# Kernel optimization log

Hardware: AMD Instinct MI355X
Metric: run time of the kernel (lower is better)

## Reference

```python
import jax, jax.numpy as jnp
import numpy as np

# Module constants from init_kwargs
A, T, HID, H, EGO = 50, 50, 128, 32, 0
C = 4 * HID // H   # per-head out channels = 16
B = 32
NEG_SLOPE = 0.2    # PyG GATConv default negative_slope


def setup_inputs() -> dict:
    key = jax.random.key(0)
    k1, k2, k3, k4 = jax.random.split(key, 4)
    h = jax.random.normal(k1, (B, A, T, HID), dtype=jnp.float32)
    # GATConv params: lin.weight (H*C, HID), att_src/att_dst (H, C), bias (H*C,)
    W = jax.random.normal(k2, (H * C, HID), dtype=jnp.float32) * (1.0 / np.sqrt(HID))
    att_src = jax.random.normal(k3, (H, C), dtype=jnp.float32) * 0.1
    att_dst = jax.random.normal(k4, (H, C), dtype=jnp.float32) * 0.1
    bias = jnp.zeros((H * C,), dtype=jnp.float32)
    return {"h": h, "W": W, "att_src": att_src, "att_dst": att_dst, "bias": bias}


def reference(h, W, att_src, att_dst, bias):
    # h: (B, A, T, HID). Node id = t*A + a after permute, matching build_ego_star_edges.
    b = h.shape[0]
    x = jnp.transpose(h, (0, 2, 1, 3))                       # (B, T, A, HID)
    # Linear projection into heads: (B, T, A, H, C)
    xw = jnp.einsum('btad,hcd->btahc', x, W.reshape(H, C, HID))
    a_src = jnp.einsum('btahc,hc->btah', xw, att_src)        # per-node src logit
    a_dst = jnp.einsum('btahc,hc->btah', xw, att_dst)        # per-node dst logit

    # Star topology: every (t_src, a != EGO) node -> every (t_dst, EGO) node.
    ne = jnp.array([a for a in range(A) if a != EGO])        # (A-1,) non-ego agents
    S = T * (A - 1)                                          # neighbors per ego dst
    x_ne = xw[:, :, ne].reshape(b, S, H, C)                  # (B, S, H, C)
    a_src_ne = a_src[:, :, ne].reshape(b, S, H)              # (B, S, H)
    a_dst_ego = a_dst[:, :, EGO]                             # (B, T, H)

    # Per-edge attention logits, segment-softmax over the S neighbors of each dst.
    logits = jax.nn.leaky_relu(a_src_ne[:, None, :, :] + a_dst_ego[:, :, None, :],
                               negative_slope=NEG_SLOPE)     # (B, T, S, H)
    att = jax.nn.softmax(logits, axis=2)

    # Weighted aggregation: (B, T, H, C) -> flatten heads (concat=True)
    out_ego = jnp.einsum('btsh,bshc->bthc', att, x_ne).reshape(b, T, H * C)

    # Nodes with no incoming edges get zero aggregation; bias added to all.
    out = jnp.zeros((b, T, A, H * C), dtype=h.dtype).at[:, :, EGO].set(out_ego)
    out = out + bias
    return jnp.transpose(out, (0, 2, 1, 3))                  # (B, A, T, H*C)
```

## Files before the change

kernel.cpp:

```cpp
#include <hip/hip_runtime.h>
#include <math.h>

#define NA    50
#define NT    50
#define HIDK  128
#define NH    32
#define NC    16
#define NB    32
#define SAT   2500
#define NS    2450
#define NOUT  512

__global__ __launch_bounds__(256) void k0_pq(const float* __restrict__ W,
                                             const float* __restrict__ att_src,
                                             const float* __restrict__ att_dst,
                                             float* __restrict__ PQ) {
  int g = blockIdx.x * 256 + threadIdx.x;
  int j = g >> 7, k = g & 127;
  int hh = j & 31;
  const float* att = (j < 32) ? att_src : att_dst;
  float acc = 0.f;
  #pragma unroll
  for (int c = 0; c < 16; ++c)
    acc = fmaf(att[hh * 16 + c], W[(size_t)(hh * 16 + c) * 128 + k], acc);
  PQ[g] = acc;
}

__global__ __launch_bounds__(256) void k1_ud(
    const float* __restrict__ X,
    const float* __restrict__ PQ,
    float* __restrict__ u,
    float* __restrict__ dv)
{
  __shared__ float Ast[32][68];
  __shared__ float Bst[32][68];
  const int tid = threadIdx.x;
  const int m0 = blockIdx.x * 64;
  const int ty = tid >> 4, tx = tid & 15;
  float acc[4][4] = {};
  const int sr = tid >> 3, sc = tid & 7;

  for (int kc = 0; kc < 128; kc += 32) {
    #pragma unroll
    for (int L = 0; L < 2; ++L) {
      int row = sr + L * 32;
      float4 v = *(const float4*)&X[(size_t)(m0 + row) * 128 + kc + sc * 4];
      Ast[sc*4+0][row] = v.x; Ast[sc*4+1][row] = v.y;
      Ast[sc*4+2][row] = v.z; Ast[sc*4+3][row] = v.w;
      float4 w = *(const float4*)&PQ[(size_t)row * 128 + kc + sc * 4];
      Bst[sc*4+0][row] = w.x; Bst[sc*4+1][row] = w.y;
      Bst[sc*4+2][row] = w.z; Bst[sc*4+3][row] = w.w;
    }
    __syncthreads();
    #pragma unroll
    for (int k = 0; k < 32; ++k) {
      float4 a4 = *(const float4*)&Ast[k][ty * 4];
      float4 b4 = *(const float4*)&Bst[k][tx * 4];
      float a[4] = {a4.x, a4.y, a4.z, a4.w};
      float bb[4] = {b4.x, b4.y, b4.z, b4.w};
      #pragma unroll
      for (int i = 0; i < 4; ++i)
        #pragma unroll
        for (int j = 0; j < 4; ++j)
          acc[i][j] = fmaf(a[i], bb[j], acc[i][j]);
    }
    __syncthreads();
  }

  #pragma unroll
  for (int i = 0; i < 4; ++i) {
    int m = m0 + ty * 4 + i;
    int b = m / SAT, s = m - b * SAT;
    #pragma unroll
    for (int jj = 0; jj < 4; ++jj) {
      int col = tx * 4 + jj;
      if (col < 32)
        u[(size_t)(b * 32 + col) * SAT + s] = acc[i][jj];
      else if (s < NT)
        dv[(size_t)(b * 32 + col - 32) * NT + s] = acc[i][jj];
    }
  }
}

#define LOADG(B_, g_) do {                                                  \
    _Pragma("unroll")                                                       \
    for (int j = 0; j < 4; ++j) {                                           \
      int idx_ = base + 2 * ((g_) * 4 + j);                                 \
      e##B_[j] = sE[idx_]; s##B_[j] = sIdx[idx_];                           \
    }                                                                       \
    _Pragma("unroll")                                                       \
    for (int j = 0; j < 4; ++j)                                             \
      x##B_[j] = *(const float4*)(xb + (size_t)s##B_[j] * HIDK);            \
  } while (0)

#define COMPG(B_) do {                                                      \
    _Pragma("unroll")                                                       \
    for (int j = 0; j < 4; ++j) {                                           \
      float2 ee = e##B_[j]; float4 xx = x##B_[j];                           \
      a1[0]=fmaf(ee.x,xx.x,a1[0]); a1[1]=fmaf(ee.x,xx.y,a1[1]);             \
      a1[2]=fmaf(ee.x,xx.z,a1[2]); a1[3]=fmaf(ee.x,xx.w,a1[3]);             \
      a2[0]=fmaf(ee.y,xx.x,a2[0]); a2[1]=fmaf(ee.y,xx.y,a2[1]);             \
      a2[2]=fmaf(ee.y,xx.z,a2[2]); a2[3]=fmaf(ee.y,xx.w,a2[3]);             \
      z1 += ee.x; z2 += ee.y;                                               \
    }                                                                       \
  } while (0)

__global__ __launch_bounds__(512, 4) void k2_attn(
    const float* __restrict__ X,
    const float* __restrict__ u,
    const float* __restrict__ dv,
    const float* __restrict__ W,
    const float* __restrict__ bias,
    float* __restrict__ out)
{
  const int id = blockIdx.x;
  const int b  = (id & 7) + 8 * (id >> 8);
  const int h  = (id >> 3) & 31;
  const int tid = threadIdx.x;

  __shared__ float Bb[2][51][129];
  __shared__ float2 sE[NS];
  __shared__ unsigned short sIdx[NS];
  __shared__ float sTheta[50], sD[50], sF1[50], sF2[50];
  __shared__ int   sRank[50];
  __shared__ int   offs[52];
  __shared__ int   offCur[51];
  __shared__ float red[8];
  __shared__ float sMaxU;

  float* sU = &Bb[0][0][0];
  unsigned short* sBeta = (unsigned short*)&Bb[1][0][0];

  const size_t bh = (size_t)b * 32 + h;
  const float* uP = u + bh * SAT + NT;

  float mx = -1e30f;
  for (int i = tid; i < NS; i += 512) { float v = uP[i]; sU[i] = v; mx = fmaxf(mx, v); }
  if (tid < 50) sD[tid] = dv[bh * NT + tid];
  if (tid < 51) offCur[tid] = 0;
  #pragma unroll
  for (int o = 32; o; o >>= 1) mx = fmaxf(mx, __shfl_xor(mx, o));
  if ((tid & 63) == 0) red[tid >> 6] = mx;
  __syncthreads();
  if (tid == 0) {
    float m2 = red[0];
    #pragma unroll
    for (int k = 1; k < 8; ++k) m2 = fmaxf(m2, red[k]);
    sMaxU = m2;
  }
  __syncthreads();
  const float maxU = sMaxU;

  if (tid < 50) {
    float th = -sD[tid];
    int r = 0;
    for (int t2 = 0; t2 < 50; ++t2) {
      float th2 = -sD[t2];
      r += (th2 < th) || (th2 == th && t2 < tid);
    }
    sRank[tid] = r;
    sTheta[r] = th;
    float x = maxU + sD[tid];
    float L = (x >= 0.f) ? x : 0.2f * x;
    sF1[tid] = __expf(x - L);
    sF2[tid] = __expf(0.2f * x - L);
  }
  __syncthreads();

  for (int i = tid; i < NS; i += 512) {
    float uu = sU[i];
    int lo = 0, hi = 50;
    while (lo < hi) { int mid = (lo + hi) >> 1; if (sTheta[mid] <= uu) lo = mid + 1; else hi = mid; }
    sBeta[i] = (unsigned short)lo;
    atomicAdd(&offCur[lo], 1);
  }
  __syncthreads();
  if (tid == 0) {
    int run = 0;
    for (int k = 0; k < 51; ++k) { int c = offCur[k]; offs[k] = run; run += c; }
    offs[51] = run;
  }
  __syncthreads();
  if (tid < 51) offCur[tid] = offs[tid];
  __syncthreads();

  for (int i = tid; i < NS; i += 512) {
    float uu = sU[i];
    int beta = sBeta[i];
    int pos = atomicAdd(&offCur[beta], 1);
    sE[pos] = make_float2(__expf(uu - maxU), __expf(0.2f * (uu - maxU)));
    sIdx[pos] = (unsigned short)(i + NT);
  }
  __syncthreads();

  {
    const int wave = tid >> 6;
    const int lane = tid & 63;
    const int slot = lane >> 5;
    const int cq   = lane & 31;
    const float* xb = X + (size_t)b * SAT * HIDK + cq * 4;

    for (int seg = wave; seg < 51; seg += 8) {
      const int i0 = offs[seg], i1 = offs[seg + 1];
      const int base = i0 + slot;
      int np = i1 - base;
      np = (np > 0) ? ((np + 1) >> 1) : 0;
      const int G = np >> 2;

      float a1[4] = {0.f, 0.f, 0.f, 0.f};
      float a2[4] = {0.f, 0.f, 0.f, 0.f};
      float z1 = 0.f, z2 = 0.f;

      float2 eA[4], eB[4]; int sA[4], sB[4]; float4 xA[4], xB[4];
      int g = 0;
      if (G) LOADG(A, 0);
      while (g + 2 <= G) {
        LOADG(B, g + 1);
        COMPG(A);
        if (g + 2 < G) LOADG(A, g + 2);
        COMPG(B);
        g += 2;
      }
      if (g < G) COMPG(A);
      for (int k = G * 4; k < np; ++k) {
        int idx = base + 2 * k;
        float2 ee = sE[idx];
        int ss = sIdx[idx];
        float4 xx = *(const float4*)(xb + (size_t)ss * HIDK);
        a1[0]=fmaf(ee.x,xx.x,a1[0]); a1[1]=fmaf(ee.x,xx.y,a1[1]);
        a1[2]=fmaf(ee.x,xx.z,a1[2]); a1[3]=fmaf(ee.x,xx.w,a1[3]);
        a2[0]=fmaf(ee.y,xx.x,a2[0]); a2[1]=fmaf(ee.y,xx.y,a2[1]);
        a2[2]=fmaf(ee.y,xx.z,a2[2]); a2[3]=fmaf(ee.y,xx.w,a2[3]);
        z1 += ee.x; z2 += ee.y;
      }

      #pragma unroll
      for (int j = 0; j < 4; ++j) {
        a1[j] += __shfl_xor(a1[j], 32);
        a2[j] += __shfl_xor(a2[j], 32);
      }
      z1 += __shfl_xor(z1, 32);
      z2 += __shfl_xor(z2, 32);
      if (slot == 0) {
        #pragma unroll
        for (int j = 0; j < 4; ++j) {
          Bb[0][seg][cq * 4 + j] = a1[j];
          Bb[1][seg][cq * 4 + j] = a2[j];
        }
        if (cq == 0) { Bb[0][seg][128] = z1; Bb[1][seg][128] = z2; }
      }
    }
  }
  __syncthreads();

  float* WshT = (float*)sE;
  const float* Wh = W + (size_t)h * 16 * 128;
  for (int v = tid; v < 2048; v += 512) {
    int k = v >> 4, cout = v & 15;
    WshT[k * 16 + cout] = Wh[(size_t)cout * 128 + k];
  }
  for (int task = tid; task < 258; task += 512) {
    int which = task >= 129;
    int c = task - which * 129;
    if (which == 0) {
      float run = 0.f;
      for (int k = 50; k >= 0; --k) { float tmp = Bb[0][k][c]; Bb[0][k][c] = run; run += tmp; }
    } else {
      float run = 0.f;
      for (int k = 0; k <= 50; ++k) { run += Bb[1][k][c]; Bb[1][k][c] = run; }
    }
  }
  __syncthreads();

  for (int task = tid; task < NT * NC; task += 512) {
    int t = task >> 4, cout = task & 15;
    int r = sRank[t];
    float F1 = sF1[t], F2 = sF2[t];
    float z = F1 * Bb[0][r][128] + F2 * Bb[1][r][128];
    const float* b1r = &Bb[0][r][0];
    const float* b2r = &Bb[1][r][0];
    float n1 = 0.f, n2 = 0.f;
    #pragma unroll 4
    for (int c = 0; c < 128; ++c) {
      float w = WshT[c * 16 + cout];
      n1 = fmaf(b1r[c], w, n1);
      n2 = fmaf(b2r[c], w, n2);
    }
    out[((size_t)b * SAT + t) * NOUT + h * 16 + cout] =
        (F1 * n1 + F2 * n2) / z + bias[h * 16 + cout];
  }

  {
    int g0 = id * 9800 + tid;
    const float4 b4 = ((const float4*)bias)[g0 & 127];
    float4* o4 = (float4*)out;
    int gEnd = (id + 1) * 9800;
    for (int g = g0; g < gEnd; g += 512) {
      int bb2 = g / 313600;
      int o = g - bb2 * 313600;
      o4[(size_t)bb2 * 320000 + 6400 + o] = b4;
    }
  }
}

extern "C" void kernel_launch(void* const* d_in, const int* in_sizes, int n_in,
                              void* d_out, int out_size, void* d_ws, size_t ws_size,
                              hipStream_t stream) {
  const float* X       = (const float*)d_in[0];
  const float* Wm      = (const float*)d_in[1];
  const float* att_src = (const float*)d_in[2];
  const float* att_dst = (const float*)d_in[3];
  const float* bias    = (const float*)d_in[4];
  float* out = (float*)d_out;

  float* PQ = (float*)d_ws;
  float* u  = PQ + 64 * 128;
  float* dv = u + (size_t)NB * NH * SAT;

  hipLaunchKernelGGL(k0_pq, dim3(32), dim3(256), 0, stream, Wm, att_src, att_dst, PQ);
  hipLaunchKernelGGL(k1_ud, dim3(1250), dim3(256), 0, stream, X, PQ, u, dv);
  hipLaunchKernelGGL(k2_attn, dim3(1024), dim3(512), 0, stream,
                     X, u, dv, Wm, bias, out);
}
```

Before: 297.1 us.

## Fuse attention-logit projection into attention kernel and parallelize offset scan

Removes the separate GEMM kernel that produced per-node source/destination logits and instead computes them inside the attention kernel. Each block dot-products its batch's node features with the head's projected attention vectors held in shared memory. This drops a kernel launch and the global round-trip for the logit buffers. In exchange, every head-block re-reads the full batch feature tensor with strided per-thread row access. The serial single-thread prefix sum over segment counts is also replaced by a wave shuffle scan.

```diff
diff --git a/kernel.cpp b/kernel.cpp
--- a/kernel.cpp
+++ b/kernel.cpp
@@ -26,62 +26,6 @@
   PQ[g] = acc;
 }
 
-__global__ __launch_bounds__(256) void k1_ud(
-    const float* __restrict__ X,
-    const float* __restrict__ PQ,
-    float* __restrict__ u,
-    float* __restrict__ dv)
-{
-  __shared__ float Ast[32][68];
-  __shared__ float Bst[32][68];
-  const int tid = threadIdx.x;
-  const int m0 = blockIdx.x * 64;
-  const int ty = tid >> 4, tx = tid & 15;
-  float acc[4][4] = {};
-  const int sr = tid >> 3, sc = tid & 7;
-
-  for (int kc = 0; kc < 128; kc += 32) {
-    #pragma unroll
-    for (int L = 0; L < 2; ++L) {
-      int row = sr + L * 32;
-      float4 v = *(const float4*)&X[(size_t)(m0 + row) * 128 + kc + sc * 4];
-      Ast[sc*4+0][row] = v.x; Ast[sc*4+1][row] = v.y;
-      Ast[sc*4+2][row] = v.z; Ast[sc*4+3][row] = v.w;
-      float4 w = *(const float4*)&PQ[(size_t)row * 128 + kc + sc * 4];
-      Bst[sc*4+0][row] = w.x; Bst[sc*4+1][row] = w.y;
-      Bst[sc*4+2][row] = w.z; Bst[sc*4+3][row] = w.w;
-    }
-    __syncthreads();
-    #pragma unroll
-    for (int k = 0; k < 32; ++k) {
-      float4 a4 = *(const float4*)&Ast[k][ty * 4];
-      float4 b4 = *(const float4*)&Bst[k][tx * 4];
-      float a[4] = {a4.x, a4.y, a4.z, a4.w};
-      float bb[4] = {b4.x, b4.y, b4.z, b4.w};
-      #pragma unroll
-      for (int i = 0; i < 4; ++i)
-        #pragma unroll
-        for (int j = 0; j < 4; ++j)
-          acc[i][j] = fmaf(a[i], bb[j], acc[i][j]);
-    }
-    __syncthreads();
-  }
-
-  #pragma unroll
-  for (int i = 0; i < 4; ++i) {
-    int m = m0 + ty * 4 + i;
-    int b = m / SAT, s = m - b * SAT;
-    #pragma unroll
-    for (int jj = 0; jj < 4; ++jj) {
-      int col = tx * 4 + jj;
-      if (col < 32)
-        u[(size_t)(b * 32 + col) * SAT + s] = acc[i][jj];
-      else if (s < NT)
-        dv[(size_t)(b * 32 + col - 32) * NT + s] = acc[i][jj];
-    }
-  }
-}
-
 #define LOADG(B_, g_) do {                                                  \
     _Pragma("unroll")                                                       \
     for (int j = 0; j < 4; ++j) {                                           \
@@ -107,8 +51,7 @@
 
 __global__ __launch_bounds__(512, 4) void k2_attn(
     const float* __restrict__ X,
-    const float* __restrict__ u,
-    const float* __restrict__ dv,
+    const float* __restrict__ PQ,
     const float* __restrict__ W,
     const float* __restrict__ bias,
     float* __restrict__ out)
@@ -121,6 +64,7 @@
   __shared__ float Bb[2][51][129];
   __shared__ float2 sE[NS];
   __shared__ unsigned short sIdx[NS];
+  __shared__ float sPQv[256];
   __shared__ float sTheta[50], sD[50], sF1[50], sF2[50];
   __shared__ int   sRank[50];
   __shared__ int   offs[52];
@@ -131,13 +75,40 @@
   float* sU = &Bb[0][0][0];
   unsigned short* sBeta = (unsigned short*)&Bb[1][0][0];
 
-  const size_t bh = (size_t)b * 32 + h;
-  const float* uP = u + bh * SAT + NT;
+  const float* Xb = X + (size_t)b * SAT * HIDK;
+
+  if (tid < 128) {
+    sPQv[tid]       = PQ[(size_t)h * 128 + tid];
+    sPQv[128 + tid] = PQ[(size_t)(32 + h) * 128 + tid];
+  }
+  if (tid < 51) offCur[tid] = 0;
+  __syncthreads();
 
   float mx = -1e30f;
-  for (int i = tid; i < NS; i += 512) { float v = uP[i]; sU[i] = v; mx = fmaxf(mx, v); }
-  if (tid < 50) sD[tid] = dv[bh * NT + tid];
-  if (tid < 51) offCur[tid] = 0;
+  {
+    const float4* p4 = (const float4*)sPQv;
+    const float4* q4 = (const float4*)(sPQv + 128);
+    #pragma unroll
+    for (int k = 0; k < 5; ++k) {
+      int row = tid + k * 512;
+      if (row < SAT) {
+        const float4* xr = (const float4*)(Xb + (size_t)row * HIDK);
+        const float4* wp = (row < NT) ? q4 : p4;
+        float4 acc4 = make_float4(0.f, 0.f, 0.f, 0.f);
+        #pragma unroll
+        for (int c4 = 0; c4 < 32; ++c4) {
+          float4 x = xr[c4], w = wp[c4];
+          acc4.x = fmaf(x.x, w.x, acc4.x);
+          acc4.y = fmaf(x.y, w.y, acc4.y);
+          acc4.z = fmaf(x.z, w.z, acc4.z);
+          acc4.w = fmaf(x.w, w.w, acc4.w);
+        }
+        float acc = (acc4.x + acc4.y) + (acc4.z + acc4.w);
+        if (row < NT) sD[row] = acc;
+        else { sU[row - NT] = acc; mx = fmaxf(mx, acc); }
+      }
+    }
+  }
   #pragma unroll
   for (int o = 32; o; o >>= 1) mx = fmaxf(mx, __shfl_xor(mx, o));
   if ((tid & 63) == 0) red[tid >> 6] = mx;
@@ -175,13 +146,18 @@
     atomicAdd(&offCur[lo], 1);
   }
   __syncthreads();
-  if (tid == 0) {
-    int run = 0;
-    for (int k = 0; k < 51; ++k) { int c = offCur[k]; offs[k] = run; run += c; }
-    offs[51] = run;
-  }
-  __syncthreads();
-  if (tid < 51) offCur[tid] = offs[tid];
+
+  if (tid < 64) {
+    int c = (tid < 51) ? offCur[tid] : 0;
+    int inc = c;
+    #pragma unroll
+    for (int o = 1; o < 64; o <<= 1) {
+      int n = __shfl_up(inc, o);
+      if (tid >= o) inc += n;
+    }
+    if (tid < 51) { int ex = inc - c; offs[tid] = ex; offCur[tid] = ex; }
+    if (tid == 50) offs[51] = inc;
+  }
   __syncthreads();
 
   for (int i = tid; i < NS; i += 512) {
@@ -198,7 +174,7 @@
     const int lane = tid & 63;
     const int slot = lane >> 5;
     const int cq   = lane & 31;
-    const float* xb = X + (size_t)b * SAT * HIDK + cq * 4;
+    const float* xb = Xb + cq * 4;
 
     for (int seg = wave; seg < 51; seg += 8) {
       const int i0 = offs[seg], i1 = offs[seg + 1];
@@ -314,11 +290,8 @@
   float* out = (float*)d_out;
 
   float* PQ = (float*)d_ws;
-  float* u  = PQ + 64 * 128;
-  float* dv = u + (size_t)NB * NH * SAT;
 
   hipLaunchKernelGGL(k0_pq, dim3(32), dim3(256), 0, stream, Wm, att_src, att_dst, PQ);
-  hipLaunchKernelGGL(k1_ud, dim3(1250), dim3(256), 0, stream, X, PQ, u, dv);
   hipLaunchKernelGGL(k2_attn, dim3(1024), dim3(512), 0, stream,
-                     X, u, dv, Wm, bias, out);
+                     X, PQ, Wm, bias, out);
 }
```

Result: slower. 450.4 us (+51.6%).

## Dynamically schedule segments largest-first across waves with a wave-parallel prefix scan

Applied to the files above, without the earlier changes.

Replaces the serial single-thread exclusive scan of segment counts with a 64-lane shuffle-based scan. Segments are ranked by size and handed out to waves through a shared atomic counter in largest-first order, replacing the static round-robin wave-to-segment assignment. This targets load imbalance when the segment sizes are skewed, at the cost of one extra O(51^2) ranking pass and an atomic per segment.

```diff
diff --git a/kernel.cpp b/kernel.cpp
--- a/kernel.cpp
+++ b/kernel.cpp
@@ -125,6 +125,8 @@
   __shared__ int   sRank[50];
   __shared__ int   offs[52];
   __shared__ int   offCur[51];
+  __shared__ int   segOrder[51];
+  __shared__ int   segCtr;
   __shared__ float red[8];
   __shared__ float sMaxU;
 
@@ -175,15 +177,30 @@
     atomicAdd(&offCur[lo], 1);
   }
   __syncthreads();
-  if (tid == 0) {
-    int run = 0;
-    for (int k = 0; k < 51; ++k) { int c = offCur[k]; offs[k] = run; run += c; }
-    offs[51] = run;
-  }
-  __syncthreads();
-  if (tid < 51) offCur[tid] = offs[tid];
-  __syncthreads();
-
+
+  if (tid < 64) {
+    int c = (tid < 51) ? offCur[tid] : 0;
+    int inc = c;
+    #pragma unroll
+    for (int o = 1; o < 64; o <<= 1) {
+      int n = __shfl_up(inc, o);
+      if (tid >= o) inc += n;
+    }
+    if (tid < 51) { int ex = inc - c; offs[tid] = ex; offCur[tid] = ex; }
+    if (tid == 50) offs[51] = inc;
+  }
+  __syncthreads();
+
+  if (tid < 51) {
+    int sz = offs[tid + 1] - offs[tid];
+    int r = 0;
+    for (int t2 = 0; t2 < 51; ++t2) {
+      int sz2 = offs[t2 + 1] - offs[t2];
+      r += (sz2 > sz) || (sz2 == sz && t2 < tid);
+    }
+    segOrder[r] = tid;
+  }
+  if (tid == 511) segCtr = 0;
   for (int i = tid; i < NS; i += 512) {
     float uu = sU[i];
     int beta = sBeta[i];
@@ -194,13 +211,18 @@
   __syncthreads();
 
   {
-    const int wave = tid >> 6;
     const int lane = tid & 63;
     const int slot = lane >> 5;
     const int cq   = lane & 31;
     const float* xb = X + (size_t)b * SAT * HIDK + cq * 4;
 
-    for (int seg = wave; seg < 51; seg += 8) {
+    for (;;) {
+      int kidx = 0;
+      if (lane == 0) kidx = atomicAdd(&segCtr, 1);
+      kidx = __shfl(kidx, 0);
+      if (kidx >= 51) break;
+      const int seg = segOrder[kidx];
+
       const int i0 = offs[seg], i1 = offs[seg + 1];
       const int base = i0 + slot;
       int np = i1 - base;
```

Result: faster. 289.6 us (median of 2 runs) (-2.5%).
